# Optimization experiments

Measured on AMD Instinct MI355X. Metric: run time of the kernel, lower is better.

The kernel has to match this reference:

```python
import jax, jax.numpy as jnp
import numpy as np

B, N = 2, 8192


def setup_inputs() -> dict:
    key = jax.random.key(0)
    ks = jax.random.split(key, 12)
    p = lambda k: jax.random.normal(k, (1, 1), jnp.float32) * 0.5
    return {
        "x": jax.random.normal(ks[0], (B, N), jnp.float32),
        "DSM": jax.random.uniform(ks[1], (N, N), jnp.float32),
        "w1": p(ks[2]), "b1": jnp.zeros((1,), jnp.float32),
        "lw1": p(ks[3]), "lb1": jnp.zeros((1,), jnp.float32),
        "lw2": p(ks[4]), "lb2": jnp.zeros((1,), jnp.float32),
        "w2": p(ks[5]), "b2": jnp.zeros((1,), jnp.float32),
        "w3": p(ks[6]), "b3": jnp.zeros((1,), jnp.float32),
        "wa": p(ks[7]), "ba": jnp.zeros((1,), jnp.float32),
        "wv": p(ks[8]), "bv": jnp.zeros((1,), jnp.float32),
    }


def _gcn_weighted(h, adj, w, b):
    # PyG GCNConv(normalize=True) on a complete graph whose edge weights are
    # adj[src, dst]; all self-loops already exist, so add_remaining_self_loops
    # is a no-op. deg[c] = sum over incoming edge weights (column sum),
    # norm[r,c] = deg[r]^-1/2 * adj[r,c] * deg[c]^-1/2, scatter-add at targets.
    deg = jnp.sum(adj, axis=0)                              # [N]
    dinv = jnp.where(deg > 0, jax.lax.rsqrt(deg), 0.0)
    anorm = dinv[:, None] * adj * dinv[None, :]             # [src, dst]
    hw = h * w[0, 0]                                        # Linear(1,1,bias=False)
    out = jnp.einsum('rc,brd->bcd', anorm, hw)              # [B,N,1]
    return out + b


def _gcn_uniform(h, w, b):
    # edge_weight=None on the complete graph: deg = N everywhere, every
    # normalized edge weight = 1/N -> output at each node is the node-mean.
    m = jnp.mean(h * w[0, 0], axis=-2, keepdims=True)       # [B,1,1]
    return jnp.broadcast_to(m, h.shape) + b


def reference(x, DSM, w1, b1, lw1, lb1, lw2, lb2, w2, b2, w3, b3, wa, ba, wv, bv):
    h = x[:, :, None]                                       # [B,N,1]
    h = jax.nn.relu(_gcn_weighted(h, DSM, w1, b1))
    h = jax.nn.relu(h * lw1[0, 0] + lb1)
    h = jax.nn.relu(h * lw2[0, 0] + lb2)
    h = jax.nn.relu(_gcn_uniform(h, w2, b2))
    h = jax.nn.relu(_gcn_uniform(h, w3, b3))
    action_prob = jax.nn.softmax(h * wa[0, 0] + ba, axis=-1)  # [B,N,1]
    u = jnp.max(h, axis=0, keepdims=True)                   # MaxAggregation dim=0
    v = jnp.max(u, axis=-2, keepdims=True)                  # MaxAggregation dim=-2
    state_values = v * wv[0, 0] + bv                        # [1,1,1]
    return action_prob, state_values
```

## Files before the change

kernel.cpp:

```cpp
#include <hip/hip_runtime.h>
#include <math.h>

#define N 8192
#define NV4 (N / 4)
#define ROWS_PER_BLOCK 64
#define GRID_X 8
#define THREADS 256


__global__ void k_colsum(const float* __restrict__ dsm, float* __restrict__ deg) {
    int chunk = (blockIdx.x + blockIdx.y) & (GRID_X - 1);
    int c4 = chunk * THREADS + threadIdx.x;
    int r0 = blockIdx.y * ROWS_PER_BLOCK;
    const float4* p = (const float4*)dsm;
    float4 acc = {0.f, 0.f, 0.f, 0.f};
#pragma unroll 8
    for (int i = 0; i < ROWS_PER_BLOCK; ++i) {
        float4 v = p[(size_t)(r0 + i) * NV4 + c4];
        acc.x += v.x; acc.y += v.y; acc.z += v.z; acc.w += v.w;
    }
    int c = c4 * 4;
    atomicAdd(&deg[c + 0], acc.x);
    atomicAdd(&deg[c + 1], acc.y);
    atomicAdd(&deg[c + 2], acc.z);
    atomicAdd(&deg[c + 3], acc.w);
}

__global__ void k_matvec(const float* __restrict__ dsm, const float* __restrict__ deg,
                         const float* __restrict__ x, float* __restrict__ t) {
    __shared__ float sg0[ROWS_PER_BLOCK];
    __shared__ float sg1[ROWS_PER_BLOCK];
    int r0 = blockIdx.y * ROWS_PER_BLOCK;
    if (threadIdx.x < ROWS_PER_BLOCK) {
        int r = r0 + threadIdx.x;
        float d = deg[r];
        float di = d > 0.f ? rsqrtf(d) : 0.f;
        sg0[threadIdx.x] = di * x[r];
        sg1[threadIdx.x] = di * x[N + r];
    }
    __syncthreads();
    int chunk = (blockIdx.x + blockIdx.y) & (GRID_X - 1);
    int c4 = chunk * THREADS + threadIdx.x;
    const float4* p = (const float4*)dsm;
    float4 a0 = {0.f, 0.f, 0.f, 0.f};
    float4 a1 = {0.f, 0.f, 0.f, 0.f};
#pragma unroll 8
    for (int i = 0; i < ROWS_PER_BLOCK; ++i) {
        float4 v = p[(size_t)(r0 + i) * NV4 + c4];
        float g0 = sg0[i], g1 = sg1[i];
        a0.x += v.x * g0; a0.y += v.y * g0; a0.z += v.z * g0; a0.w += v.w * g0;
        a1.x += v.x * g1; a1.y += v.y * g1; a1.z += v.z * g1; a1.w += v.w * g1;
    }
    int c = c4 * 4;
    atomicAdd(&t[c + 0], a0.x);
    atomicAdd(&t[c + 1], a0.y);
    atomicAdd(&t[c + 2], a0.z);
    atomicAdd(&t[c + 3], a0.w);
    atomicAdd(&t[N + c + 0], a1.x);
    atomicAdd(&t[N + c + 1], a1.y);
    atomicAdd(&t[N + c + 2], a1.z);
    atomicAdd(&t[N + c + 3], a1.w);
}

__global__ void k_head(const float* __restrict__ t, const float* __restrict__ deg,
                       const float* __restrict__ w1, const float* __restrict__ b1,
                       const float* __restrict__ lw1, const float* __restrict__ lb1,
                       const float* __restrict__ lw2, const float* __restrict__ lb2,
                       float* __restrict__ msum, float* __restrict__ out) {
    int c = blockIdx.x * THREADS + threadIdx.x;
    float W1 = w1[0], B1 = b1[0];
    float LW1 = lw1[0], LB1 = lb1[0];
    float LW2 = lw2[0], LB2 = lb2[0];
    float d = deg[c];
    float di = d > 0.f ? rsqrtf(d) : 0.f;
    float v0, v1;
    {
        float h = W1 * di * t[c] + B1;
        h = fmaxf(h, 0.f);
        h = fmaxf(h * LW1 + LB1, 0.f);
        v0 = fmaxf(h * LW2 + LB2, 0.f);
    }
    {
        float h = W1 * di * t[N + c] + B1;
        h = fmaxf(h, 0.f);
        h = fmaxf(h * LW1 + LB1, 0.f);
        v1 = fmaxf(h * LW2 + LB2, 0.f);
    }
    out[c] = 1.0f;
    out[N + c] = 1.0f;
    for (int off = 32; off > 0; off >>= 1) {
        v0 += __shfl_down(v0, off);
        v1 += __shfl_down(v1, off);
    }
    if ((threadIdx.x & 63) == 0) {
        atomicAdd(&msum[0], v0);
        atomicAdd(&msum[1], v1);
    }
}

__global__ void k_out(const float* __restrict__ msum,
                      const float* __restrict__ w2, const float* __restrict__ b2,
                      const float* __restrict__ w3, const float* __restrict__ b3,
                      const float* __restrict__ wv, const float* __restrict__ bv,
                      float* __restrict__ out) {
    float vmax = -INFINITY;
    for (int b = 0; b < 2; ++b) {
        float m = msum[b] * (1.0f / (float)N);
        float s = fmaxf(m * w2[0] + b2[0], 0.f);
        s = fmaxf(s * w3[0] + b3[0], 0.f);
        vmax = fmaxf(vmax, s);
    }
    out[2 * N] = vmax * wv[0] + bv[0];
}

extern "C" void kernel_launch(void* const* d_in, const int* in_sizes, int n_in,
                              void* d_out, int out_size, void* d_ws, size_t ws_size,
                              hipStream_t stream) {
    const float* x   = (const float*)d_in[0];
    const float* dsm = (const float*)d_in[1];
    const float* w1  = (const float*)d_in[2];
    const float* b1  = (const float*)d_in[3];
    const float* lw1 = (const float*)d_in[4];
    const float* lb1 = (const float*)d_in[5];
    const float* lw2 = (const float*)d_in[6];
    const float* lb2 = (const float*)d_in[7];
    const float* w2  = (const float*)d_in[8];
    const float* b2  = (const float*)d_in[9];
    const float* w3  = (const float*)d_in[10];
    const float* b3  = (const float*)d_in[11];
    const float* wv  = (const float*)d_in[14];
    const float* bv  = (const float*)d_in[15];

    float* ws   = (float*)d_ws;
    float* deg  = ws;
    float* t    = ws + N;
    float* msum = ws + 3 * N;

    hipMemsetAsync(deg, 0, (3 * N + 2) * sizeof(float), stream);

    dim3 big(GRID_X, N / ROWS_PER_BLOCK);
    k_colsum<<<big, THREADS, 0, stream>>>(dsm, deg);
    k_matvec<<<big, THREADS, 0, stream>>>(dsm, deg, x, t);
    k_head<<<N / THREADS, THREADS, 0, stream>>>(t, deg, w1, b1, lw1, lb1, lw2, lb2,
                                                msum, (float*)d_out);
    k_out<<<1, 1, 0, stream>>>(msum, w2, b2, w3, b3, wv, bv, (float*)d_out);
}
```

Measured before the change: 443.7 us.

## Replace global atomics with per-block partial buffers and hierarchical reductions

```diff
diff --git a/kernel.cpp b/kernel.cpp
--- a/kernel.cpp
+++ b/kernel.cpp
@@ -3,114 +3,138 @@
 
 #define N 8192
 #define NV4 (N / 4)
-#define ROWS_PER_BLOCK 64
+#define RPB 64
+#define NBY (N / RPB)
 #define GRID_X 8
 #define THREADS 256
 
+#define DEGP_OFF  0
+#define TPART_OFF (NBY * N)
+#define HPART_OFF (TPART_OFF + NBY * 2 * N)
 
-__global__ void k_colsum(const float* __restrict__ dsm, float* __restrict__ deg) {
+__global__ void k_colsum(const float* __restrict__ dsm, float* __restrict__ degp) {
     int chunk = (blockIdx.x + blockIdx.y) & (GRID_X - 1);
     int c4 = chunk * THREADS + threadIdx.x;
-    int r0 = blockIdx.y * ROWS_PER_BLOCK;
+    int r0 = blockIdx.y * RPB;
     const float4* p = (const float4*)dsm;
     float4 acc = {0.f, 0.f, 0.f, 0.f};
-#pragma unroll 8
-    for (int i = 0; i < ROWS_PER_BLOCK; ++i) {
+#pragma unroll 16
+    for (int i = 0; i < RPB; ++i) {
         float4 v = p[(size_t)(r0 + i) * NV4 + c4];
         acc.x += v.x; acc.y += v.y; acc.z += v.z; acc.w += v.w;
     }
-    int c = c4 * 4;
-    atomicAdd(&deg[c + 0], acc.x);
-    atomicAdd(&deg[c + 1], acc.y);
-    atomicAdd(&deg[c + 2], acc.z);
-    atomicAdd(&deg[c + 3], acc.w);
+    ((float4*)(degp + (size_t)blockIdx.y * N))[c4] = acc;
 }
 
-__global__ void k_matvec(const float* __restrict__ dsm, const float* __restrict__ deg,
-                         const float* __restrict__ x, float* __restrict__ t) {
-    __shared__ float sg0[ROWS_PER_BLOCK];
-    __shared__ float sg1[ROWS_PER_BLOCK];
-    int r0 = blockIdx.y * ROWS_PER_BLOCK;
-    if (threadIdx.x < ROWS_PER_BLOCK) {
-        int r = r0 + threadIdx.x;
-        float d = deg[r];
-        float di = d > 0.f ? rsqrtf(d) : 0.f;
-        sg0[threadIdx.x] = di * x[r];
-        sg1[threadIdx.x] = di * x[N + r];
+__global__ void k_matvec(const float* __restrict__ dsm, const float* __restrict__ degp,
+                         const float* __restrict__ x, float* __restrict__ tpart) {
+    __shared__ float sred[4 * RPB];
+    __shared__ float sg0[RPB];
+    __shared__ float sg1[RPB];
+    int r0 = blockIdx.y * RPB;
+
+    {
+        int rl = threadIdx.x & 63;
+        int q  = threadIdx.x >> 6;
+        const float* dp = degp + r0 + rl;
+        float s = 0.f;
+#pragma unroll 8
+        for (int j = 0; j < 32; ++j) s += dp[(size_t)(q * 32 + j) * N];
+        sred[q * RPB + rl] = s;
     }
     __syncthreads();
+    if (threadIdx.x < RPB) {
+        int r = threadIdx.x;
+        float d = sred[r] + sred[RPB + r] + sred[2 * RPB + r] + sred[3 * RPB + r];
+        float di = d > 0.f ? rsqrtf(d) : 0.f;
+        sg0[r] = di * x[r0 + r];
+        sg1[r] = di * x[N + r0 + r];
+    }
+    __syncthreads();
+
     int chunk = (blockIdx.x + blockIdx.y) & (GRID_X - 1);
     int c4 = chunk * THREADS + threadIdx.x;
     const float4* p = (const float4*)dsm;
     float4 a0 = {0.f, 0.f, 0.f, 0.f};
     float4 a1 = {0.f, 0.f, 0.f, 0.f};
-#pragma unroll 8
-    for (int i = 0; i < ROWS_PER_BLOCK; ++i) {
+#pragma unroll 16
+    for (int i = 0; i < RPB; ++i) {
         float4 v = p[(size_t)(r0 + i) * NV4 + c4];
         float g0 = sg0[i], g1 = sg1[i];
         a0.x += v.x * g0; a0.y += v.y * g0; a0.z += v.z * g0; a0.w += v.w * g0;
         a1.x += v.x * g1; a1.y += v.y * g1; a1.z += v.z * g1; a1.w += v.w * g1;
     }
-    int c = c4 * 4;
-    atomicAdd(&t[c + 0], a0.x);
-    atomicAdd(&t[c + 1], a0.y);
-    atomicAdd(&t[c + 2], a0.z);
-    atomicAdd(&t[c + 3], a0.w);
-    atomicAdd(&t[N + c + 0], a1.x);
-    atomicAdd(&t[N + c + 1], a1.y);
-    atomicAdd(&t[N + c + 2], a1.z);
-    atomicAdd(&t[N + c + 3], a1.w);
+    ((float4*)(tpart + ((size_t)blockIdx.y * 2 + 0) * N))[c4] = a0;
+    ((float4*)(tpart + ((size_t)blockIdx.y * 2 + 1) * N))[c4] = a1;
 }
 
-__global__ void k_head(const float* __restrict__ t, const float* __restrict__ deg,
+__global__ void k_head(const float* __restrict__ degp, const float* __restrict__ tpart,
                        const float* __restrict__ w1, const float* __restrict__ b1,
                        const float* __restrict__ lw1, const float* __restrict__ lb1,
                        const float* __restrict__ lw2, const float* __restrict__ lb2,
-                       float* __restrict__ msum, float* __restrict__ out) {
+                       float* __restrict__ hpart, float* __restrict__ out) {
+    __shared__ float swred[8];
     int c = blockIdx.x * THREADS + threadIdx.x;
+
+    float d = 0.f, t0 = 0.f, t1 = 0.f;
+#pragma unroll 8
+    for (int by = 0; by < NBY; ++by) {
+        d  += degp[(size_t)by * N + c];
+        t0 += tpart[((size_t)by * 2 + 0) * N + c];
+        t1 += tpart[((size_t)by * 2 + 1) * N + c];
+    }
+    float di = d > 0.f ? rsqrtf(d) : 0.f;
+
     float W1 = w1[0], B1 = b1[0];
     float LW1 = lw1[0], LB1 = lb1[0];
     float LW2 = lw2[0], LB2 = lb2[0];
-    float d = deg[c];
-    float di = d > 0.f ? rsqrtf(d) : 0.f;
-    float v0, v1;
-    {
-        float h = W1 * di * t[c] + B1;
-        h = fmaxf(h, 0.f);
-        h = fmaxf(h * LW1 + LB1, 0.f);
-        v0 = fmaxf(h * LW2 + LB2, 0.f);
-    }
-    {
-        float h = W1 * di * t[N + c] + B1;
-        h = fmaxf(h, 0.f);
-        h = fmaxf(h * LW1 + LB1, 0.f);
-        v1 = fmaxf(h * LW2 + LB2, 0.f);
-    }
+    float h0 = fmaxf(W1 * di * t0 + B1, 0.f);
+    h0 = fmaxf(h0 * LW1 + LB1, 0.f);
+    h0 = fmaxf(h0 * LW2 + LB2, 0.f);
+    float h1 = fmaxf(W1 * di * t1 + B1, 0.f);
+    h1 = fmaxf(h1 * LW1 + LB1, 0.f);
+    h1 = fmaxf(h1 * LW2 + LB2, 0.f);
+
     out[c] = 1.0f;
     out[N + c] = 1.0f;
+
+    float v0 = h0, v1 = h1;
     for (int off = 32; off > 0; off >>= 1) {
         v0 += __shfl_down(v0, off);
         v1 += __shfl_down(v1, off);
     }
-    if ((threadIdx.x & 63) == 0) {
-        atomicAdd(&msum[0], v0);
-        atomicAdd(&msum[1], v1);
+    int wave = threadIdx.x >> 6;
+    if ((threadIdx.x & 63) == 0) { swred[wave] = v0; swred[4 + wave] = v1; }
+    __syncthreads();
+    if (threadIdx.x == 0) {
+        hpart[blockIdx.x * 2 + 0] = swred[0] + swred[1] + swred[2] + swred[3];
+        hpart[blockIdx.x * 2 + 1] = swred[4] + swred[5] + swred[6] + swred[7];
     }
 }
 
-__global__ void k_out(const float* __restrict__ msum,
+__global__ void k_out(const float* __restrict__ hpart,
                       const float* __restrict__ w2, const float* __restrict__ b2,
                       const float* __restrict__ w3, const float* __restrict__ b3,
                       const float* __restrict__ wv, const float* __restrict__ bv,
                       float* __restrict__ out) {
-    float vmax = -INFINITY;
-    for (int b = 0; b < 2; ++b) {
-        float m = msum[b] * (1.0f / (float)N);
-        float s = fmaxf(m * w2[0] + b2[0], 0.f);
-        s = fmaxf(s * w3[0] + b3[0], 0.f);
-        vmax = fmaxf(vmax, s);
+    int tid = threadIdx.x;
+    float s0 = tid < 32 ? hpart[tid * 2 + 0] : 0.f;
+    float s1 = tid < 32 ? hpart[tid * 2 + 1] : 0.f;
+    for (int off = 16; off > 0; off >>= 1) {
+        s0 += __shfl_down(s0, off);
+        s1 += __shfl_down(s1, off);
     }
-    out[2 * N] = vmax * wv[0] + bv[0];
+    if (tid == 0) {
+        float vmax = -INFINITY;
+        float m0 = s0 * (1.0f / (float)N);
+        float m1 = s1 * (1.0f / (float)N);
+        float a = fmaxf(m0 * w2[0] + b2[0], 0.f);
+        a = fmaxf(a * w3[0] + b3[0], 0.f);
+        float b = fmaxf(m1 * w2[0] + b2[0], 0.f);
+        b = fmaxf(b * w3[0] + b3[0], 0.f);
+        vmax = fmaxf(a, b);
+        out[2 * N] = vmax * wv[0] + bv[0];
+    }
 }
 
 extern "C" void kernel_launch(void* const* d_in, const int* in_sizes, int n_in,
@@ -131,17 +155,15 @@
     const float* wv  = (const float*)d_in[14];
     const float* bv  = (const float*)d_in[15];
 
-    float* ws   = (float*)d_ws;
-    float* deg  = ws;
-    float* t    = ws + N;
-    float* msum = ws + 3 * N;
+    float* ws    = (float*)d_ws;
+    float* degp  = ws + DEGP_OFF;
+    float* tpart = ws + TPART_OFF;
+    float* hpart = ws + HPART_OFF;
 
-    hipMemsetAsync(deg, 0, (3 * N + 2) * sizeof(float), stream);
-
-    dim3 big(GRID_X, N / ROWS_PER_BLOCK);
-    k_colsum<<<big, THREADS, 0, stream>>>(dsm, deg);
-    k_matvec<<<big, THREADS, 0, stream>>>(dsm, deg, x, t);
-    k_head<<<N / THREADS, THREADS, 0, stream>>>(t, deg, w1, b1, lw1, lb1, lw2, lb2,
-                                                msum, (float*)d_out);
-    k_out<<<1, 1, 0, stream>>>(msum, w2, b2, w3, b3, wv, bv, (float*)d_out);
+    dim3 big(GRID_X, NBY);
+    k_colsum<<<big, THREADS, 0, stream>>>(dsm, degp);
+    k_matvec<<<big, THREADS, 0, stream>>>(dsm, degp, x, tpart);
+    k_head<<<N / THREADS, THREADS, 0, stream>>>(degp, tpart, w1, b1, lw1, lb1,
+                                                lw2, lb2, hpart, (float*)d_out);
+    k_out<<<1, 64, 0, stream>>>(hpart, w2, b2, w3, b3, wv, bv, (float*)d_out);
 }
```

After: 439.5 us. Within noise of the previous version (-1.0%).
